# Kernel tuning notes

Hardware: AMD Instinct MI355X
Metric: run time of the kernel (lower is better)

## Reference

```python
import jax, jax.numpy as jnp
import numpy as np

BN_EPS = 1e-5


def _binarize_act(x):
    # sign(x) forward, clipped STE backward (grad passes where |x|<1)
    xc = jnp.clip(x, -1.0, 1.0)
    return xc + jax.lax.stop_gradient(jnp.sign(x) - xc)


def _binarize_weight(w):
    # XNOR/ReActNet: per-out-channel scale * sign(w); clipped-STE gradient
    scale = jax.lax.stop_gradient(jnp.mean(jnp.abs(w), axis=(1, 2, 3), keepdims=True))
    wc = jnp.clip(w, -1.0, 1.0)
    return wc + jax.lax.stop_gradient(scale * jnp.sign(w) - wc)


def setup_inputs() -> dict:
    key = jax.random.key(0)
    ks = jax.random.split(key, 8)
    B, C, H, W = 64, 64, 56, 56
    P = 64  # planes == inplanes (stride 1, no downsample)
    x = jax.random.normal(ks[0], (B, C, H, W), dtype=jnp.float32)
    bias0 = jnp.zeros((1, C, 1, 1), dtype=jnp.float32)
    w = jax.random.normal(ks[1], (P, C, 3, 3), dtype=jnp.float32) * 0.1
    gamma = jnp.ones((P,), dtype=jnp.float32)
    beta = jnp.zeros((P,), dtype=jnp.float32)
    run_mean = jax.random.normal(ks[2], (P,), dtype=jnp.float32) * 0.1
    run_var = jax.random.uniform(ks[3], (P,), dtype=jnp.float32, minval=0.5, maxval=1.5)
    bias1 = jnp.zeros((1, P, 1, 1), dtype=jnp.float32)
    alpha = jnp.full((P,), 0.25, dtype=jnp.float32)  # PReLU default init
    bias2 = jnp.zeros((1, P, 1, 1), dtype=jnp.float32)
    return {"x": x, "bias0": bias0, "w": w, "gamma": gamma, "beta": beta,
            "run_mean": run_mean, "run_var": run_var, "bias1": bias1,
            "alpha": alpha, "bias2": bias2}


def reference(x, bias0, w, gamma, beta, run_mean, run_var, bias1, alpha, bias2):
    residual = x
    out = x + bias0                      # move0 (LearnableBias)
    out = _binarize_act(out)             # BinAct: sign, clipped STE
    bw = _binarize_weight(w)             # BinConv weight binarization
    out = jax.lax.conv_general_dilated(
        out, bw, window_strides=(1, 1), padding=((1, 1), (1, 1)),
        dimension_numbers=("NCHW", "OIHW", "NCHW"))
    # BatchNorm2d (inference form with running stats)
    inv = gamma / jnp.sqrt(run_var + BN_EPS)
    out = out * inv[None, :, None, None] + (beta - run_mean * inv)[None, :, None, None]
    out = out + residual                 # residual add (downsample is None)
    out = out + bias1                    # move1
    a = alpha[None, :, None, None]
    out = jnp.where(out >= 0, out, a * out)  # PReLU
    out = out + bias2                    # move2
    return out
```

## Files before the change

### kernel.cpp

```cpp
#include <hip/hip_runtime.h>

typedef unsigned long long u64;
typedef unsigned int u32;

#define BATCH 64
#define CH    64
#define HH    56
#define WW    56
#define HW    3136
#define SROW  64
#define SIMG  (58 * SROW)
#define PBLK  896

__global__ __launch_bounds__(256)
void pack_kernel(const float* __restrict__ x,
                 const float* __restrict__ bias0,
                 const float* __restrict__ w,
                 const float* __restrict__ gamma,
                 const float* __restrict__ beta,
                 const float* __restrict__ rmean,
                 const float* __restrict__ rvar,
                 const float* __restrict__ bias1,
                 const float* __restrict__ alpha,
                 const float* __restrict__ bias2,
                 u64* __restrict__ Spk,
                 u64* __restrict__ wtab,
                 float* __restrict__ kc) {
    const int tid = threadIdx.x;
    const int lane = tid & 63;
    const int wv = tid >> 6;
    const int blk = blockIdx.x;

    if (blk < PBLK) {
        const int row = blk * 4 + wv;
        const int b = row / HH;
        const int h = row - b * HH;
        const float* xp = x + ((size_t)(b * CH + lane)) * HW + h * WW;
        const float bz = bias0[lane];
        u64 mine = 0;
#pragma unroll
        for (int q = 0; q < 14; ++q) {
            float4 v = *(const float4*)(xp + q * 4);
            u64 m0 = __ballot(v.x + bz > 0.f);
            u64 m1 = __ballot(v.y + bz > 0.f);
            u64 m2 = __ballot(v.z + bz > 0.f);
            u64 m3 = __ballot(v.w + bz > 0.f);
            mine = (lane == q * 4 + 0) ? m0 : mine;
            mine = (lane == q * 4 + 1) ? m1 : mine;
            mine = (lane == q * 4 + 2) ? m2 : mine;
            mine = (lane == q * 4 + 3) ? m3 : mine;
        }
        u64* sp = Spk + (size_t)b * SIMG + (h + 1) * SROW;
        if (lane < WW)           sp[1 + lane] = mine;
        else if (lane == 56)     sp[0] = 0;
        else if (lane == 57)     sp[57] = 0;
        if (h == 0 && lane < 58)      Spk[(size_t)b * SIMG + lane] = 0;
        if (h == HH - 1 && lane < 58) Spk[(size_t)b * SIMG + 57 * SROW + lane] = 0;
    } else {
        __shared__ float red[4];
        const int p = blk - PBLK;
        const float* wp = w + p * 576;
        float s = 0.f;
        for (int i = tid; i < 576; i += 256) s += fabsf(wp[i]);
#pragma unroll
        for (int off = 32; off > 0; off >>= 1) s += __shfl_down(s, off);
        if (lane == 0) red[wv] = s;
        __syncthreads();

        if (wv == 0) {
            u64 m[9];
#pragma unroll
            for (int t = 0; t < 9; ++t) {
                m[t] = __ballot(wp[lane * 9 + t] > 0.f);
                if (lane == 0) wtab[p * 12 + t] = m[t];
            }
            if (lane == 0) {
                float scale = (red[0] + red[1] + red[2] + red[3]) * (1.0f / 576.0f);
                float inv = gamma[p] * rsqrtf(rvar[p] + 1e-5f);
                float am = scale * inv;
                float bd = beta[p] - rmean[p] * inv + bias1[p];
                float pt[9];
#pragma unroll
                for (int t = 0; t < 9; ++t) pt[t] = (float)__popcll(m[t]);
                const float cL = pt[0] + pt[3] + pt[6];
                const float cR = pt[2] + pt[5] + pt[8];
                const float rT = pt[0] + pt[1] + pt[2];
                const float rB = pt[6] + pt[7] + pt[8];
                float Ci[3][3] = {
                    {0.f, cL,                 cR},
                    {rT,  rT + pt[3] + pt[6], rT + pt[5] + pt[8]},
                    {rB,  rB + pt[0] + pt[3], rB + pt[2] + pt[5]}};
                float nv[3][3] = {{9, 6, 6}, {6, 4, 4}, {6, 4, 4}};
#pragma unroll
                for (int wc = 0; wc < 3; ++wc)
#pragma unroll
                    for (int lc = 0; lc < 3; ++lc)
                        kc[(wc * 3 + lc) * 64 + p] =
                            fmaf(am, 64.f * nv[wc][lc] + 2.f * Ci[wc][lc], bd);
                float* wf = (float*)(wtab + p * 12 + 9);
                wf[0] = -2.f * am;
                wf[1] = alpha[p];
                wf[2] = bias2[p];
                wf[3] = 0.f;
            }
        }
    }
}

__global__ __launch_bounds__(256, 6)
void conv_kernel(const u64* __restrict__ Spk,
                 const u64* __restrict__ wtab,
                 const float* __restrict__ kc,
                 const float* __restrict__ x,
                 float* __restrict__ out) {
    __shared__ float kcsm[576];
    const int tid = threadIdx.x;
    for (int i = tid; i < 576; i += 256) kcsm[i] = kc[i];
    __syncthreads();

    const int bid = blockIdx.x;
    const int wg = (bid & 7) * 224 + (bid >> 3);
    const int lane = tid & 63;
    const int wvu = __builtin_amdgcn_readfirstlane(tid >> 6);
    const int row = wg * 2 + (wvu & 1);
    const int ph = (wvu >> 1) << 5;
    const int b = row / HH;
    const int h = row - b * HH;
    const int wl = min(lane, WW - 1);
    const bool active = lane < WW;

    const u64* ap = Spk + (size_t)b * SIMG + (h + 1) * SROW + (wl + 1);
    u64 a0 = ap[-SROW - 1], a1 = ap[-SROW], a2 = ap[-SROW + 1];
    u64 a3 = ap[-1],        a4 = ap[0],     a5 = ap[1];
    u64 a6 = ap[SROW - 1],  a7 = ap[SROW],  a8 = ap[SROW + 1];

    const int wclass = (h == 0) ? 1 : (h == HH - 1) ? 2 : 0;
    const int lclass = (lane == 0) ? 1 : (lane == WW - 1) ? 2 : 0;
    const float* kp = kcsm + (wclass * 3 + lclass) * 64 + ph;

    size_t off = (size_t)b * CH * HW + (size_t)h * WW + wl + (size_t)ph * HW;
    const u64* wp = wtab + (size_t)ph * 12;

#pragma unroll 2
    for (int i = 0; i < 32; ++i) {
        u32 P = 0;
        u64 v;
        v = a0 ^ wp[0]; P += __popc((u32)v); P += __popc((u32)(v >> 32));
        v = a1 ^ wp[1]; P += __popc((u32)v); P += __popc((u32)(v >> 32));
        v = a2 ^ wp[2]; P += __popc((u32)v); P += __popc((u32)(v >> 32));
        v = a3 ^ wp[3]; P += __popc((u32)v); P += __popc((u32)(v >> 32));
        v = a4 ^ wp[4]; P += __popc((u32)v); P += __popc((u32)(v >> 32));
        v = a5 ^ wp[5]; P += __popc((u32)v); P += __popc((u32)(v >> 32));
        v = a6 ^ wp[6]; P += __popc((u32)v); P += __popc((u32)(v >> 32));
        v = a7 ^ wp[7]; P += __popc((u32)v); P += __popc((u32)(v >> 32));
        v = a8 ^ wp[8]; P += __popc((u32)v); P += __popc((u32)(v >> 32));

        const float* cf = (const float*)(wp + 9);
        const float k = kp[i];
        const float res = x[off];
        float o = fmaf(cf[0], (float)P, k) + res;
        o = o >= 0.f ? o : cf[1] * o;
        o += cf[2];
        if (active) out[off] = o;

        off += HW;
        wp += 12;
    }
}

extern "C" void kernel_launch(void* const* d_in, const int* in_sizes, int n_in,
                              void* d_out, int out_size, void* d_ws, size_t ws_size,
                              hipStream_t stream) {
    const float* x     = (const float*)d_in[0];
    const float* bias0 = (const float*)d_in[1];
    const float* w     = (const float*)d_in[2];
    const float* gamma = (const float*)d_in[3];
    const float* beta  = (const float*)d_in[4];
    const float* rmean = (const float*)d_in[5];
    const float* rvar  = (const float*)d_in[6];
    const float* bias1 = (const float*)d_in[7];
    const float* alpha = (const float*)d_in[8];
    const float* bias2 = (const float*)d_in[9];
    float* out = (float*)d_out;

    char* ws = (char*)d_ws;
    u64* wtab = (u64*)ws;
    float* kc = (float*)(ws + 6144);
    u64* Spk  = (u64*)(ws + 16384);

    pack_kernel<<<PBLK + 64, 256, 0, stream>>>(
        x, bias0, w, gamma, beta, rmean, rvar, bias1, alpha, bias2,
        Spk, wtab, kc);

    conv_kernel<<<(BATCH * HH) / 2, 256, 0, stream>>>(Spk, wtab, kc, x, out);
}
```

Baseline: 44.22 us.

## Merge per-channel constants into weight records and double-buffer residual loads

New measurement: 59.39 us. 1.34x slower.

```diff
diff --git a/kernel.cpp b/kernel.cpp
--- a/kernel.cpp
+++ b/kernel.cpp
@@ -24,8 +24,7 @@
                  const float* __restrict__ alpha,
                  const float* __restrict__ bias2,
                  u64* __restrict__ Spk,
-                 u64* __restrict__ wtab,
-                 float* __restrict__ kc) {
+                 u64* __restrict__ wtab) {
     const int tid = threadIdx.x;
     const int lane = tid & 63;
     const int wv = tid >> 6;
@@ -69,10 +68,11 @@
 
         if (wv == 0) {
             u64 m[9];
+            u64* rec = wtab + p * 16;
 #pragma unroll
             for (int t = 0; t < 9; ++t) {
                 m[t] = __ballot(wp[lane * 9 + t] > 0.f);
-                if (lane == 0) wtab[p * 12 + t] = m[t];
+                if (lane == 0) rec[t] = m[t];
             }
             if (lane == 0) {
                 float scale = (red[0] + red[1] + red[2] + red[3]) * (1.0f / 576.0f);
@@ -91,33 +91,29 @@
                     {rT,  rT + pt[3] + pt[6], rT + pt[5] + pt[8]},
                     {rB,  rB + pt[0] + pt[3], rB + pt[2] + pt[5]}};
                 float nv[3][3] = {{9, 6, 6}, {6, 4, 4}, {6, 4, 4}};
+                float* kf = (float*)(rec + 9);
 #pragma unroll
                 for (int wc = 0; wc < 3; ++wc)
 #pragma unroll
                     for (int lc = 0; lc < 3; ++lc)
-                        kc[(wc * 3 + lc) * 64 + p] =
+                        kf[wc * 3 + lc] =
                             fmaf(am, 64.f * nv[wc][lc] + 2.f * Ci[wc][lc], bd);
-                float* wf = (float*)(wtab + p * 12 + 9);
-                wf[0] = -2.f * am;
-                wf[1] = alpha[p];
-                wf[2] = bias2[p];
-                wf[3] = 0.f;
+                kf[9]  = -2.f * am;
+                kf[10] = alpha[p];
+                kf[11] = bias2[p];
+                kf[12] = 0.f;
+                kf[13] = 0.f;
             }
         }
     }
 }
 
-__global__ __launch_bounds__(256, 6)
+__global__ __launch_bounds__(256, 8)
 void conv_kernel(const u64* __restrict__ Spk,
                  const u64* __restrict__ wtab,
-                 const float* __restrict__ kc,
                  const float* __restrict__ x,
                  float* __restrict__ out) {
-    __shared__ float kcsm[576];
     const int tid = threadIdx.x;
-    for (int i = tid; i < 576; i += 256) kcsm[i] = kc[i];
-    __syncthreads();
-
     const int bid = blockIdx.x;
     const int wg = (bid & 7) * 224 + (bid >> 3);
     const int lane = tid & 63;
@@ -130,41 +126,60 @@
     const bool active = lane < WW;
 
     const u64* ap = Spk + (size_t)b * SIMG + (h + 1) * SROW + (wl + 1);
-    u64 a0 = ap[-SROW - 1], a1 = ap[-SROW], a2 = ap[-SROW + 1];
-    u64 a3 = ap[-1],        a4 = ap[0],     a5 = ap[1];
-    u64 a6 = ap[SROW - 1],  a7 = ap[SROW],  a8 = ap[SROW + 1];
-
-    const int wclass = (h == 0) ? 1 : (h == HH - 1) ? 2 : 0;
-    const int lclass = (lane == 0) ? 1 : (lane == WW - 1) ? 2 : 0;
-    const float* kp = kcsm + (wclass * 3 + lclass) * 64 + ph;
-
-    size_t off = (size_t)b * CH * HW + (size_t)h * WW + wl + (size_t)ph * HW;
-    const u64* wp = wtab + (size_t)ph * 12;
-
-#pragma unroll 2
-    for (int i = 0; i < 32; ++i) {
-        u32 P = 0;
-        u64 v;
-        v = a0 ^ wp[0]; P += __popc((u32)v); P += __popc((u32)(v >> 32));
-        v = a1 ^ wp[1]; P += __popc((u32)v); P += __popc((u32)(v >> 32));
-        v = a2 ^ wp[2]; P += __popc((u32)v); P += __popc((u32)(v >> 32));
-        v = a3 ^ wp[3]; P += __popc((u32)v); P += __popc((u32)(v >> 32));
-        v = a4 ^ wp[4]; P += __popc((u32)v); P += __popc((u32)(v >> 32));
-        v = a5 ^ wp[5]; P += __popc((u32)v); P += __popc((u32)(v >> 32));
-        v = a6 ^ wp[6]; P += __popc((u32)v); P += __popc((u32)(v >> 32));
-        v = a7 ^ wp[7]; P += __popc((u32)v); P += __popc((u32)(v >> 32));
-        v = a8 ^ wp[8]; P += __popc((u32)v); P += __popc((u32)(v >> 32));
-
-        const float* cf = (const float*)(wp + 9);
-        const float k = kp[i];
-        const float res = x[off];
-        float o = fmaf(cf[0], (float)P, k) + res;
-        o = o >= 0.f ? o : cf[1] * o;
-        o += cf[2];
-        if (active) out[off] = o;
-
-        off += HW;
-        wp += 12;
+    u64 A0 = ap[-SROW - 1], A1 = ap[-SROW], A2 = ap[-SROW + 1];
+    u64 A3 = ap[-1],        A4 = ap[0],     A5 = ap[1];
+    u64 A6 = ap[SROW - 1],  A7 = ap[SROW],  A8 = ap[SROW + 1];
+    asm volatile("" : "+v"(A0), "+v"(A1), "+v"(A2), "+v"(A3), "+v"(A4),
+                      "+v"(A5), "+v"(A6), "+v"(A7), "+v"(A8));
+
+    const int wc3 = (h == 0) ? 3 : (h == HH - 1) ? 6 : 0;
+    const bool isL = (lane == 0);
+    const bool isR = (lane == WW - 1);
+
+    const u32 base = (u32)(b * CH * HW + h * WW + wl) + (u32)ph * HW;
+
+    float res[2][8];
+#pragma unroll
+    for (int j = 0; j < 8; ++j) res[0][j] = x[base + (u32)j * HW];
+#pragma unroll
+    for (int j = 0; j < 8; ++j) asm volatile("" : "+v"(res[0][j]));
+
+    u32 off = base;
+#pragma unroll
+    for (int c = 0; c < 4; ++c) {
+        if (c < 3) {
+#pragma unroll
+            for (int j = 0; j < 8; ++j)
+                res[(c + 1) & 1][j] = x[base + (u32)((c + 1) * 8 + j) * HW];
+#pragma unroll
+            for (int j = 0; j < 8; ++j)
+                asm volatile("" : "+v"(res[(c + 1) & 1][j]));
+        }
+
+#pragma unroll
+        for (int j = 0; j < 8; ++j) {
+            const u64* wp = wtab + (ph + c * 8 + j) * 16;
+            u32 P0 = 0, P1 = 0;
+            u64 v;
+            v = A0 ^ wp[0]; P0 += __popc((u32)v); P1 += __popc((u32)(v >> 32));
+            v = A1 ^ wp[1]; P0 += __popc((u32)v); P1 += __popc((u32)(v >> 32));
+            v = A2 ^ wp[2]; P0 += __popc((u32)v); P1 += __popc((u32)(v >> 32));
+            v = A3 ^ wp[3]; P0 += __popc((u32)v); P1 += __popc((u32)(v >> 32));
+            v = A4 ^ wp[4]; P0 += __popc((u32)v); P1 += __popc((u32)(v >> 32));
+            v = A5 ^ wp[5]; P0 += __popc((u32)v); P1 += __popc((u32)(v >> 32));
+            v = A6 ^ wp[6]; P0 += __popc((u32)v); P1 += __popc((u32)(v >> 32));
+            v = A7 ^ wp[7]; P0 += __popc((u32)v); P1 += __popc((u32)(v >> 32));
+            v = A8 ^ wp[8]; P0 += __popc((u32)v); P1 += __popc((u32)(v >> 32));
+
+            const float* kf = (const float*)(wp + 9);
+            float k = isL ? kf[wc3 + 1] : kf[wc3];
+            k = isR ? kf[wc3 + 2] : k;
+            float o = fmaf(kf[9], (float)(P0 + P1), k) + res[c & 1][j];
+            o = o >= 0.f ? o : kf[10] * o;
+            o += kf[11];
+            if (active) out[off] = o;
+            off += HW;
+        }
     }
 }
 
@@ -185,12 +200,11 @@
 
     char* ws = (char*)d_ws;
     u64* wtab = (u64*)ws;
-    float* kc = (float*)(ws + 6144);
     u64* Spk  = (u64*)(ws + 16384);
 
     pack_kernel<<<PBLK + 64, 256, 0, stream>>>(
         x, bias0, w, gamma, beta, rmean, rvar, bias1, alpha, bias2,
-        Spk, wtab, kc);
-
-    conv_kernel<<<(BATCH * HH) / 2, 256, 0, stream>>>(Spk, wtab, kc, x, out);
+        Spk, wtab);
+
+    conv_kernel<<<(BATCH * HH) / 2, 256, 0, stream>>>(Spk, wtab, x, out);
 }
```
